# Kernel optimization log

Hardware: AMD Instinct MI355X
Metric: run time of the kernel (lower is better)

The kernel has to match this reference:

```python
import jax, jax.numpy as jnp
import numpy as np

D_MODEL = 192
D_STATE = 16
D_CONV = 3
EXPAND = 2
D_INNER = EXPAND * D_MODEL  # 384
DT_RANK = (D_MODEL + 15) // 16  # 12
K = 4  # scan directions
B, H, W = 2, 64, 64
EPS = 1e-5


def silu(x):
    return x * jax.nn.sigmoid(x)


def setup_inputs() -> dict:
    key = jax.random.key(0)
    ks = jax.random.split(key, 12)
    s = 0.02
    x = jax.random.normal(ks[0], (B, H, W, D_MODEL), dtype=jnp.float32)
    in_proj_w = jax.random.normal(ks[1], (2 * D_INNER, D_MODEL), dtype=jnp.float32) * s
    conv_w = jax.random.normal(ks[2], (D_INNER, 1, D_CONV, D_CONV), dtype=jnp.float32) * 0.1
    conv_b = jnp.zeros((D_INNER,), dtype=jnp.float32)
    x_proj_weight = jax.random.normal(ks[3], (K, DT_RANK + 2 * D_STATE, D_INNER), dtype=jnp.float32) * s
    dt_projs_weight = jax.random.normal(ks[4], (K, D_INNER, DT_RANK), dtype=jnp.float32) * (DT_RANK ** -0.5)
    dt_projs_bias = jax.random.uniform(ks[5], (K, D_INNER), dtype=jnp.float32, minval=-4.0, maxval=-2.0)
    # Mamba-style S4D-real init: A_n = n, stored as log
    A_logs = jnp.log(jnp.tile(jnp.arange(1, D_STATE + 1, dtype=jnp.float32), (K * D_INNER, 1)))
    Ds = jnp.ones((K * D_INNER,), dtype=jnp.float32)
    ln_gamma = jnp.ones((D_INNER,), dtype=jnp.float32)
    ln_beta = jnp.zeros((D_INNER,), dtype=jnp.float32)
    out_proj_w = jax.random.normal(ks[6], (D_MODEL, D_INNER), dtype=jnp.float32) * s
    return dict(x=x, in_proj_w=in_proj_w, conv_w=conv_w, conv_b=conv_b,
                x_proj_weight=x_proj_weight, dt_projs_weight=dt_projs_weight,
                dt_projs_bias=dt_projs_bias, A_logs=A_logs, Ds=Ds,
                ln_gamma=ln_gamma, ln_beta=ln_beta, out_proj_w=out_proj_w)


def _ss2d_forward(x, in_proj_w, conv_w, conv_b, x_proj_weight, dt_projs_weight,
                  dt_projs_bias, A_logs, Ds, ln_gamma, ln_beta, out_proj_w):
    b, h, w, _ = x.shape
    L = h * w
    # in_proj + gate split
    xz = jnp.einsum('bhwc,dc->bhwd', x, in_proj_w)  # (B,H,W,2*D_INNER)
    xc, z = jnp.split(xz, 2, axis=-1)
    # depthwise conv2d (NCHW) + SiLU
    xc = jnp.transpose(xc, (0, 3, 1, 2))  # (B,D_INNER,H,W)
    xc = jax.lax.conv_general_dilated(
        xc, conv_w, window_strides=(1, 1), padding=((1, 1), (1, 1)),
        feature_group_count=D_INNER, dimension_numbers=('NCHW', 'OIHW', 'NCHW'))
    xc = silu(xc + conv_b[None, :, None, None])
    # ---- cross-scan: 4 directions ----
    x_flat = xc.reshape(b, D_INNER, L)                                # HW order
    x_t = jnp.transpose(xc, (0, 1, 3, 2)).reshape(b, D_INNER, L)      # WH order
    xs = jnp.stack([x_flat, x_t], axis=1)                             # (B,2,D,L)
    xs = jnp.concatenate([xs, jnp.flip(xs, axis=-1)], axis=1)         # (B,4,D,L)
    # input-dependent projections
    x_dbl = jnp.einsum('bkdl,kcd->bkcl', xs, x_proj_weight)
    dts = x_dbl[:, :, :DT_RANK]
    Bmat = x_dbl[:, :, DT_RANK:DT_RANK + D_STATE]                     # (B,4,N,L)
    Cmat = x_dbl[:, :, DT_RANK + D_STATE:]                            # (B,4,N,L)
    dts = jnp.einsum('bkrl,kdr->bkdl', dts, dt_projs_weight)          # (B,4,D,L)
    delta = jax.nn.softplus(dts + dt_projs_bias[None, :, :, None])
    A = -jnp.exp(A_logs).reshape(K, D_INNER, D_STATE)                 # (4,D,N)
    # ---- selective scan over L (time-major) ----
    u_t = jnp.transpose(xs, (3, 0, 1, 2))        # (L,B,4,D)
    d_t = jnp.transpose(delta, (3, 0, 1, 2))     # (L,B,4,D)
    B_t = jnp.transpose(Bmat, (3, 0, 1, 2))      # (L,B,4,N)
    C_t = jnp.transpose(Cmat, (3, 0, 1, 2))      # (L,B,4,N)

    def step(hst, inp):
        d, bm, cm, uu = inp                       # (B,4,D) / (B,4,N)
        dA = jnp.exp(d[..., None] * A[None])      # (B,4,D,N)
        dBu = (d * uu)[..., None] * bm[:, :, None, :]
        hst = dA * hst + dBu
        y = jnp.einsum('bkdn,bkn->bkd', hst, cm)
        return hst, y

    h0 = jnp.zeros((b, K, D_INNER, D_STATE), dtype=x.dtype)
    _, ys = jax.lax.scan(step, h0, (d_t, B_t, C_t, u_t))              # (L,B,4,D)
    ys = jnp.transpose(ys, (1, 2, 3, 0))                              # (B,4,D,L)
    ys = ys + xs * Ds.reshape(K, D_INNER)[None, :, :, None]
    # ---- cross-merge ----
    y1 = ys[:, 0]
    inv2 = jnp.flip(ys[:, 2], axis=-1)
    wh = jnp.transpose(ys[:, 1].reshape(b, D_INNER, w, h), (0, 1, 3, 2)).reshape(b, D_INNER, L)
    invwh = jnp.transpose(jnp.flip(ys[:, 3], axis=-1).reshape(b, D_INNER, w, h), (0, 1, 3, 2)).reshape(b, D_INNER, L)
    y = y1 + inv2 + wh + invwh                                        # (B,D,L)
    y = jnp.transpose(y, (0, 2, 1)).reshape(b, h, w, D_INNER)
    # LayerNorm over channel
    mu = jnp.mean(y, axis=-1, keepdims=True)
    var = jnp.var(y, axis=-1, keepdims=True)
    y = (y - mu) * jax.lax.rsqrt(var + EPS) * ln_gamma + ln_beta
    # gate + out_proj
    y = y * silu(z)
    return jnp.einsum('bhwd,cd->bhwc', y, out_proj_w)


def reference(x, in_proj_w, conv_w, conv_b, x_proj_weight, dt_projs_weight,
              dt_projs_bias, A_logs, Ds, ln_gamma, ln_beta, out_proj_w):
    return _ss2d_forward(x, in_proj_w, conv_w, conv_b, x_proj_weight,
                         dt_projs_weight, dt_projs_bias, A_logs, Ds,
                         ln_gamma, ln_beta, out_proj_w)
```

## Files before the change

### kernel.cpp

```cpp
#include <hip/hip_runtime.h>
#include <cstddef>
#include <cstdint>

#define L 4096
#define DI 384
#define NDIR 4
#define NST 16
#define NCH 128
#define LCH 32
#define DTR 12

typedef __attribute__((ext_vector_type(8))) short bf16x8;
typedef __attribute__((ext_vector_type(4))) float f32x4;
typedef __attribute__((ext_vector_type(2))) float f32x2;

__device__ __forceinline__ unsigned short f2bf(float f) {
  unsigned u = __float_as_uint(f);
  u = u + 0x7fffu + ((u >> 16) & 1u);
  return (unsigned short)(u >> 16);
}
__device__ __forceinline__ float bf2f(unsigned short s) {
  return __uint_as_float(((unsigned)s) << 16);
}

__global__ __launch_bounds__(256) void cvt_all(
    const float* __restrict__ x, const float* __restrict__ ipw,
    const float* __restrict__ xpw, const float* __restrict__ opw,
    unsigned short* __restrict__ xb, unsigned short* __restrict__ ib,
    unsigned short* __restrict__ pb, unsigned short* __restrict__ ob) {
  int g = blockIdx.x * 256 + threadIdx.x;
  const float* src;
  unsigned short* dst;
  int idx;
  if (g < 393216) { src = x; dst = xb; idx = g; }
  else if (g < 430080) { src = ipw; dst = ib; idx = g - 393216; }
  else if (g < 446976) { src = xpw; dst = pb; idx = g - 430080; }
  else { src = opw; dst = ob; idx = g - 446976; }
  float4 v = *(const float4*)(src + (size_t)idx * 4);
  *(uint2*)(dst + (size_t)idx * 4) = make_uint2(
      (unsigned)f2bf(v.x) | ((unsigned)f2bf(v.y) << 16),
      (unsigned)f2bf(v.z) | ((unsigned)f2bf(v.w) << 16));
}

__global__ __launch_bounds__(256) void inproj_mfma(
    const unsigned short* __restrict__ A, const unsigned short* __restrict__ Bw,
    unsigned short* __restrict__ xc, unsigned short* __restrict__ z) {
  __shared__ unsigned short As[128 * 64];
  __shared__ unsigned short Bs[64 * 64];
  const int tid = threadIdx.x;
  const int m0 = blockIdx.x << 7;
  const int n0 = blockIdx.y << 6;
  const int lr = tid >> 4;
  const int lc = (tid & 15) << 2;
  const int wid = tid >> 6;
  const int lane = tid & 63;
  const int wr = wid >> 1, wc = wid & 1;
  const int Kdim = 192;
  f32x4 acc[4][2] = {};
  for (int k0 = 0; k0 < Kdim; k0 += 64) {
    if (k0) __syncthreads();
#pragma unroll
    for (int rr = 0; rr < 8; ++rr) {
      int r = lr + (rr << 4);
      uint2 v = *(const uint2*)(A + (size_t)(m0 + r) * Kdim + k0 + lc);
      unsigned off = ((unsigned)(r * 128 + lc * 2)) ^ ((r & 7) << 4);
      *(uint2*)((char*)As + off) = v;
    }
#pragma unroll
    for (int rr = 0; rr < 4; ++rr) {
      int r = lr + (rr << 4);
      uint2 v = *(const uint2*)(Bw + (size_t)(n0 + r) * Kdim + k0 + lc);
      unsigned off = ((unsigned)(r * 128 + lc * 2)) ^ ((r & 7) << 4);
      *(uint2*)((char*)Bs + off) = v;
    }
    __syncthreads();
#pragma unroll
    for (int kt = 0; kt < 2; ++kt) {
      const int kb = (kt << 6) + ((lane >> 4) << 4);
      bf16x8 af[4], bfr[2];
#pragma unroll
      for (int fr = 0; fr < 4; ++fr) {
        int row = (wr << 6) + (fr << 4) + (lane & 15);
        unsigned off = ((unsigned)(row * 128 + kb)) ^ ((row & 7) << 4);
        af[fr] = *(const bf16x8*)((const char*)As + off);
      }
#pragma unroll
      for (int fc = 0; fc < 2; ++fc) {
        int row = (wc << 5) + (fc << 4) + (lane & 15);
        unsigned off = ((unsigned)(row * 128 + kb)) ^ ((row & 7) << 4);
        bfr[fc] = *(const bf16x8*)((const char*)Bs + off);
      }
#pragma unroll
      for (int fr = 0; fr < 4; ++fr)
#pragma unroll
        for (int fc = 0; fc < 2; ++fc)
          acc[fr][fc] = __builtin_amdgcn_mfma_f32_16x16x32_bf16(af[fr], bfr[fc], acc[fr][fc], 0, 0, 0);
    }
  }
  const int rbase = (lane >> 4) << 2;
  const int cbase = lane & 15;
#pragma unroll
  for (int fr = 0; fr < 4; ++fr) {
#pragma unroll
    for (int fc = 0; fc < 2; ++fc) {
      int col = n0 + (wc << 5) + (fc << 4) + cbase;
      unsigned short* dst = xc;
      int cc = col;
      if (col >= 384) { dst = z; cc = col - 384; }
#pragma unroll
      for (int i = 0; i < 4; ++i) {
        int row = m0 + (wr << 6) + (fr << 4) + rbase + i;
        dst[(size_t)row * 384 + cc] = f2bf(acc[fr][fc][i]);
      }
    }
  }
}

__global__ __launch_bounds__(256) void gemm_nt_mfma_bfA(
    const unsigned short* __restrict__ A, const unsigned short* __restrict__ Bw,
    float* __restrict__ out0, int Kdim, int Ntot) {
  __shared__ unsigned short As[128 * 64];
  __shared__ unsigned short Bs[64 * 64];
  const int tid = threadIdx.x;
  const int m0 = blockIdx.x << 7;
  const int n0 = blockIdx.y << 6;
  const int lr = tid >> 4;
  const int lc = (tid & 15) << 2;
  const int wid = tid >> 6;
  const int lane = tid & 63;
  const int wr = wid >> 1, wc = wid & 1;
  f32x4 acc[4][2] = {};
  for (int k0 = 0; k0 < Kdim; k0 += 64) {
    if (k0) __syncthreads();
#pragma unroll
    for (int rr = 0; rr < 8; ++rr) {
      int r = lr + (rr << 4);
      uint2 v = *(const uint2*)(A + (size_t)(m0 + r) * Kdim + k0 + lc);
      unsigned off = ((unsigned)(r * 128 + lc * 2)) ^ ((r & 7) << 4);
      *(uint2*)((char*)As + off) = v;
    }
#pragma unroll
    for (int rr = 0; rr < 4; ++rr) {
      int r = lr + (rr << 4);
      uint2 v = *(const uint2*)(Bw + (size_t)(n0 + r) * Kdim + k0 + lc);
      unsigned off = ((unsigned)(r * 128 + lc * 2)) ^ ((r & 7) << 4);
      *(uint2*)((char*)Bs + off) = v;
    }
    __syncthreads();
#pragma unroll
    for (int kt = 0; kt < 2; ++kt) {
      const int kb = (kt << 6) + ((lane >> 4) << 4);
      bf16x8 af[4], bfr[2];
#pragma unroll
      for (int fr = 0; fr < 4; ++fr) {
        int row = (wr << 6) + (fr << 4) + (lane & 15);
        unsigned off = ((unsigned)(row * 128 + kb)) ^ ((row & 7) << 4);
        af[fr] = *(const bf16x8*)((const char*)As + off);
      }
#pragma unroll
      for (int fc = 0; fc < 2; ++fc) {
        int row = (wc << 5) + (fc << 4) + (lane & 15);
        unsigned off = ((unsigned)(row * 128 + kb)) ^ ((row & 7) << 4);
        bfr[fc] = *(const bf16x8*)((const char*)Bs + off);
      }
#pragma unroll
      for (int fr = 0; fr < 4; ++fr)
#pragma unroll
        for (int fc = 0; fc < 2; ++fc)
          acc[fr][fc] = __builtin_amdgcn_mfma_f32_16x16x32_bf16(af[fr], bfr[fc], acc[fr][fc], 0, 0, 0);
    }
  }
  const int rbase = (lane >> 4) << 2;
  const int cbase = lane & 15;
#pragma unroll
  for (int fr = 0; fr < 4; ++fr) {
#pragma unroll
    for (int fc = 0; fc < 2; ++fc) {
      int col = n0 + (wc << 5) + (fc << 4) + cbase;
#pragma unroll
      for (int i = 0; i < 4; ++i) {
        int row = m0 + (wr << 6) + (fr << 4) + rbase + i;
        out0[(size_t)row * Ntot + col] = acc[fr][fc][i];
      }
    }
  }
}

__global__ __launch_bounds__(384) void conv_silu(
    const unsigned short* __restrict__ xc_pre, const float* __restrict__ conv_w,
    const float* __restrict__ conv_b, unsigned short* __restrict__ xc_act,
    unsigned short* __restrict__ xc_act_t) {
  const int d = threadIdx.x;
  float w[9];
#pragma unroll
  for (int j = 0; j < 9; ++j) w[j] = conv_w[d * 9 + j];
  const float bias = conv_b[d];
  const int base = blockIdx.x << 2;
#pragma unroll
  for (int t = 0; t < 4; ++t) {
    int g = base + t;
    int b = g >> 12;
    int hw = g & 4095;
    int h = hw >> 6, ww = hw & 63;
    float s = bias;
#pragma unroll
    for (int ky = 0; ky < 3; ++ky) {
      int hh = h + ky - 1;
      if (hh < 0 || hh > 63) continue;
#pragma unroll
      for (int kx = 0; kx < 3; ++kx) {
        int wc = ww + kx - 1;
        if (wc < 0 || wc > 63) continue;
        s += w[ky * 3 + kx] * bf2f(xc_pre[((size_t)(b << 12) + (hh << 6) + wc) * DI + d]);
      }
    }
    float va = s / (1.f + __expf(-s));
    unsigned short vb = f2bf(va);
    xc_act[(size_t)g * DI + d] = vb;
    xc_act_t[((size_t)(b << 12) + (ww << 6) + h) * DI + d] = vb;
  }
}

__global__ __launch_bounds__(256) void xdbl_mfma(
    const unsigned short* __restrict__ xc_act, const unsigned short* __restrict__ xc_act_t,
    const unsigned short* __restrict__ xpw, float* __restrict__ xdbl) {
  __shared__ unsigned short As[128 * 64];
  __shared__ unsigned short Bs[48 * 64];
  const int tid = threadIdx.x;
  const int k = blockIdx.y, b = blockIdx.z;
  const int l0 = blockIdx.x << 7;
  const int bk = b * NDIR + k;
  const int lr = tid >> 4;
  const int lc = (tid & 15) << 2;
  const int wid = tid >> 6;
  const int lane = tid & 63;
  const unsigned short* usrc = (k & 1) ? xc_act_t : xc_act;
  const unsigned short* wbase = xpw + (size_t)k * 44 * DI;
  f32x4 acc[2][3] = {};
  for (int k0 = 0; k0 < DI; k0 += 64) {
    if (k0) __syncthreads();
#pragma unroll
    for (int rr = 0; rr < 8; ++rr) {
      int r = lr + (rr << 4);
      int l = l0 + r;
      int ll = (k & 2) ? (L - 1 - l) : l;
      uint2 v = *(const uint2*)(usrc + ((size_t)(b << 12) + ll) * DI + k0 + lc);
      unsigned off = ((unsigned)(r * 128 + lc * 2)) ^ ((r & 7) << 4);
      *(uint2*)((char*)As + off) = v;
    }
#pragma unroll
    for (int rr = 0; rr < 3; ++rr) {
      int r = lr + (rr << 4);
      uint2 v = make_uint2(0u, 0u);
      if (r < 44) v = *(const uint2*)(wbase + (size_t)r * DI + k0 + lc);
      unsigned off = ((unsigned)(r * 128 + lc * 2)) ^ ((r & 7) << 4);
      *(uint2*)((char*)Bs + off) = v;
    }
    __syncthreads();
#pragma unroll
    for (int kt = 0; kt < 2; ++kt) {
      const int kb = (kt << 6) + ((lane >> 4) << 4);
      bf16x8 af[2], bfr[3];
#pragma unroll
      for (int fr = 0; fr < 2; ++fr) {
        int row = (wid << 5) + (fr << 4) + (lane & 15);
        unsigned off = ((unsigned)(row * 128 + kb)) ^ ((row & 7) << 4);
        af[fr] = *(const bf16x8*)((const char*)As + off);
      }
#pragma unroll
      for (int nf = 0; nf < 3; ++nf) {
        int row = (nf << 4) + (lane & 15);
        unsigned off = ((unsigned)(row * 128 + kb)) ^ ((row & 7) << 4);
        bfr[nf] = *(const bf16x8*)((const char*)Bs + off);
      }
#pragma unroll
      for (int fr = 0; fr < 2; ++fr)
#pragma unroll
        for (int nf = 0; nf < 3; ++nf)
          acc[fr][nf] = __builtin_amdgcn_mfma_f32_16x16x32_bf16(af[fr], bfr[nf], acc[fr][nf], 0, 0, 0);
    }
  }
  const int rbase = (lane >> 4) << 2;
  const int cbase = lane & 15;
#pragma unroll
  for (int fr = 0; fr < 2; ++fr) {
#pragma unroll
    for (int nf = 0; nf < 3; ++nf) {
      int n = (nf << 4) + cbase;
#pragma unroll
      for (int i = 0; i < 4; ++i) {
        int row = l0 + (wid << 5) + (fr << 4) + rbase + i;
        xdbl[((size_t)bk * L + row) * 48 + n] = acc[fr][nf][i];
      }
    }
  }
}

__device__ __forceinline__ float delta_dot2(const float* __restrict__ Xrow,
                                            const f32x2* w2, float bias) {
  f32x2 acc = {bias, 0.f};
#pragma unroll
  for (int r = 0; r < 6; ++r) {
    f32x2 t = *(const f32x2*)(Xrow + 2 * r);
    acc = t * w2[r] + acc;
  }
  return acc.x + acc.y;
}

__device__ __forceinline__ void h_update4(f32x4* h4, const float* __restrict__ Brow,
                                          float p, float du) {
  float q2 = p * p, q4 = q2 * q2, q8 = q4 * q4;
  f32x4 e0;
  e0.x = p; e0.y = q2; e0.z = q2 * p; e0.w = q4;
  f32x4 e1 = e0 * q4, e2 = e0 * q8, e3 = e1 * q8;
  f32x4 B0 = *(const f32x4*)(Brow);
  f32x4 B1 = *(const f32x4*)(Brow + 4);
  f32x4 B2 = *(const f32x4*)(Brow + 8);
  f32x4 B3 = *(const f32x4*)(Brow + 12);
  h4[0] = e0 * h4[0] + du * B0;
  h4[1] = e1 * h4[1] + du * B1;
  h4[2] = e2 * h4[2] + du * B2;
  h4[3] = e3 * h4[3] + du * B3;
}

__global__ __launch_bounds__(192, 6) void scan_p1(
    const float* __restrict__ xdbl, const unsigned short* __restrict__ xc_act,
    const unsigned short* __restrict__ xc_act_t,
    const float* __restrict__ dtw, const float* __restrict__ dtb,
    unsigned short* __restrict__ ch_h, float* __restrict__ ch_sd,
    _Float16* __restrict__ cum, unsigned short* __restrict__ y_sc) {
  const int dh = blockIdx.z & 1;
  const int b = blockIdx.z >> 1;
  const int d = threadIdx.x + (dh ? 192 : 0);
  const int c = blockIdx.x, k = blockIdx.y;
  const int bk = b * NDIR + k;
  const float* xrow = xdbl + ((size_t)bk * L + c * LCH) * 48;
  f32x2 w2[6];
#pragma unroll
  for (int r = 0; r < 6; ++r) w2[r] = *(const f32x2*)(dtw + ((size_t)k * DI + d) * DTR + 2 * r);
  const float bias = dtb[k * DI + d];
  const unsigned short* usrc = (k & 1) ? xc_act_t : xc_act;
  const int ll0 = (k & 2) ? (L - 1 - c * LCH) : (c * LCH);
  const ptrdiff_t ustride = (k & 2) ? -(ptrdiff_t)DI : (ptrdiff_t)DI;
  const unsigned short* uptr = usrc + ((size_t)(b << 12) + ll0) * DI + d;
  _Float16* cbase = cum + ((size_t)bk * L + c * LCH) * DI + d;
  unsigned short* ybase = y_sc + ((size_t)bk * L + c * LCH) * DI + d;
  f32x4 h4[4] = {};
  float sd = 0.f;
  for (int g = 0; g < LCH; g += 4) {
    float du[4], p[4], dv4[4];
#pragma unroll
    for (int j = 0; j < 4; ++j) {
      int i = g + j;
      float a = delta_dot2(xrow + i * 48, w2, bias);
      float e = __expf(a);
      float dv = (a > 15.f) ? a : __logf(1.f + e);
      float u = bf2f(uptr[(ptrdiff_t)i * ustride]);
      dv4[j] = dv;
      p[j] = __builtin_amdgcn_rcpf(1.f + e);
      du[j] = dv * u;
    }
#pragma unroll
    for (int j = 0; j < 4; ++j) {
      int i = g + j;
      sd += dv4[j];
      cbase[(size_t)i * DI] = (_Float16)sd;
      h_update4(h4, xrow + i * 48 + DTR, p[j], du[j]);
      const float* Crow = xrow + i * 48 + DTR + NST;
      f32x4 y4 = h4[0] * (*(const f32x4*)(Crow));
      y4 = h4[1] * (*(const f32x4*)(Crow + 4)) + y4;
      y4 = h4[2] * (*(const f32x4*)(Crow + 8)) + y4;
      y4 = h4[3] * (*(const f32x4*)(Crow + 12)) + y4;
      ybase[(size_t)i * DI] = f2bf((y4.x + y4.y) + (y4.z + y4.w));
    }
  }
  size_t o = ((size_t)bk * NCH + c) * DI + d;
  ch_sd[o] = sd;
  const float* hf = (const float*)h4;
  unsigned wpk[8];
#pragma unroll
  for (int j = 0; j < 8; ++j)
    wpk[j] = (unsigned)f2bf(hf[2 * j]) | ((unsigned)f2bf(hf[2 * j + 1]) << 16);
  *(uint4*)(ch_h + o * 16) = make_uint4(wpk[0], wpk[1], wpk[2], wpk[3]);
  *(uint4*)(ch_h + o * 16 + 8) = make_uint4(wpk[4], wpk[5], wpk[6], wpk[7]);
}

__global__ __launch_bounds__(256) void scan_p2(
    const unsigned short* __restrict__ ch_h, const float* __restrict__ ch_sd,
    unsigned short* __restrict__ h0) {
  const int t = threadIdx.x;
  const int n = t & 15;
  const int dl = (t >> 4) & 3;
  const int seg = t >> 6;
  const int dg = blockIdx.x % 96;
  const int bk = blockIdx.x / 96;
  const int d = dg * 4 + dl;
  const float an = -(float)(n + 1);
  const int c0 = seg * 32;
  float carry = 0.f;
  float sdsum = 0.f;
  for (int i = 0; i < 32; ++i) {
    size_t o = ((size_t)bk * NCH + c0 + i) * DI + d;
    float sd = ch_sd[o];
    float hh = bf2f(ch_h[o * 16 + n]);
    carry = fmaf(__expf(an * sd), carry, hh);
    sdsum += sd;
  }
  __shared__ float sH[256], sS[256];
  sH[t] = carry;
  sS[t] = sdsum;
  __syncthreads();
  float E = 0.f;
  const int base = t & 63;
  for (int s = 0; s < seg; ++s) {
    float Rp = __expf(an * sS[base + 64 * s]);
    E = fmaf(Rp, E, sH[base + 64 * s]);
  }
  carry = E;
  for (int i = 0; i < 32; ++i) {
    size_t o = ((size_t)bk * NCH + c0 + i) * DI + d;
    float sd = ch_sd[o];
    float hh = bf2f(ch_h[o * 16 + n]);
    h0[o * 16 + n] = f2bf(carry);
    carry = fmaf(__expf(an * sd), carry, hh);
  }
}

__global__ __launch_bounds__(384) void merge_ln(
    const unsigned short* __restrict__ y_sc, const unsigned short* __restrict__ xc_act,
    const float* __restrict__ xdbl, const _Float16* __restrict__ cum,
    const unsigned short* __restrict__ h0,
    const float* __restrict__ Ds, const float* __restrict__ gamma,
    const float* __restrict__ beta, const unsigned short* __restrict__ z,
    unsigned short* __restrict__ y_gb) {
  const int d = threadIdx.x;
  const int g = blockIdx.x;
  const int b = g >> 12;
  const int hw = g & 4095;
  const int l1 = ((hw & 63) << 6) | (hw >> 6);
  const int ls[4] = {hw, l1, L - 1 - hw, L - 1 - l1};
  float v = 0.f;
#pragma unroll
  for (int k = 0; k < 4; ++k) {
    const int bk = b * NDIR + k;
    const int lk = ls[k];
    const size_t rowi = (size_t)bk * L + lk;
    float yl = bf2f(y_sc[rowi * DI + d]);
    float cs = (float)cum[rowi * DI + d];
    const float* Crow = xdbl + rowi * 48 + DTR + NST;
    const int c = lk >> 5;
    f32x4 hv[4];
    {
      const unsigned* hp = (const unsigned*)h0 + (((size_t)bk * NCH + c) * DI + d) * 8;
      float* hf = (float*)hv;
#pragma unroll
      for (int j = 0; j < 8; ++j) {
        unsigned u = hp[j];
        hf[2 * j] = bf2f((unsigned short)(u & 0xffffu));
        hf[2 * j + 1] = bf2f((unsigned short)(u >> 16));
      }
    }
    float q1 = __expf(-cs);
    float q2 = q1 * q1, q4 = q2 * q2, q8 = q4 * q4;
    f32x4 e0;
    e0.x = q1; e0.y = q2; e0.z = q2 * q1; e0.w = q4;
    f32x4 e1 = e0 * q4, e2 = e0 * q8, e3 = e1 * q8;
    f32x4 yv = (e0 * hv[0]) * (*(const f32x4*)(Crow));
    yv = (e1 * hv[1]) * (*(const f32x4*)(Crow + 4)) + yv;
    yv = (e2 * hv[2]) * (*(const f32x4*)(Crow + 8)) + yv;
    yv = (e3 * hv[3]) * (*(const f32x4*)(Crow + 12)) + yv;
    v += yl + ((yv.x + yv.y) + (yv.z + yv.w));
  }
  float u = bf2f(xc_act[(size_t)g * DI + d]);
  v += u * (Ds[d] + Ds[DI + d] + Ds[2 * DI + d] + Ds[3 * DI + d]);
  float s1 = v, s2 = v * v;
#pragma unroll
  for (int m = 1; m < 64; m <<= 1) {
    s1 += __shfl_xor(s1, m);
    s2 += __shfl_xor(s2, m);
  }
  __shared__ float r1[6], r2[6];
  const int lane = d & 63, wid = d >> 6;
  if (lane == 0) { r1[wid] = s1; r2[wid] = s2; }
  __syncthreads();
  float t1 = 0.f, t2 = 0.f;
#pragma unroll
  for (int wq = 0; wq < 6; ++wq) { t1 += r1[wq]; t2 += r2[wq]; }
  const float mu = t1 * (1.f / 384.f);
  const float var = t2 * (1.f / 384.f) - mu * mu;
  float yn = (v - mu) * rsqrtf(var + 1e-5f) * gamma[d] + beta[d];
  float zv = bf2f(z[(size_t)g * DI + d]);
  y_gb[(size_t)g * DI + d] = f2bf(yn * (zv / (1.f + __expf(-zv))));
}

extern "C" void kernel_launch(void* const* d_in, const int* in_sizes, int n_in,
                              void* d_out, int out_size, void* d_ws, size_t ws_size,
                              hipStream_t stream) {
  (void)in_sizes; (void)n_in; (void)out_size; (void)ws_size;
  const float* x      = (const float*)d_in[0];
  const float* ipw    = (const float*)d_in[1];
  const float* convw  = (const float*)d_in[2];
  const float* convb  = (const float*)d_in[3];
  const float* xpw    = (const float*)d_in[4];
  const float* dtw    = (const float*)d_in[5];
  const float* dtb    = (const float*)d_in[6];
  const float* Ds     = (const float*)d_in[8];
  const float* gamma  = (const float*)d_in[9];
  const float* beta   = (const float*)d_in[10];
  const float* opw    = (const float*)d_in[11];
  float* out = (float*)d_out;

  float* ws = (float*)d_ws;
  unsigned short* xc_pre   = (unsigned short*)ws;
  unsigned short* zbuf     = (unsigned short*)(ws + 1572864ull);
  unsigned short* xc_act   = (unsigned short*)(ws + 3145728ull);
  unsigned short* xc_act_t = (unsigned short*)(ws + 4718592ull);
  float* xdbl     = ws + 6291456ull;
  unsigned short* y_sc = (unsigned short*)(ws + 7864320ull);
  unsigned short* ch_h = (unsigned short*)(ws + 14155776ull);
  unsigned short* h0   = (unsigned short*)(ws + 17301504ull);
  float* ch_sd    = ws + 20447232ull;
  unsigned short* x_bf   = (unsigned short*)(ws + 20840448ull);
  unsigned short* ipw_bf = (unsigned short*)(ws + 21626880ull);
  unsigned short* xpw_bf = (unsigned short*)(ws + 21700608ull);
  unsigned short* opw_bf = (unsigned short*)(ws + 21734400ull);
  _Float16* cum   = (_Float16*)(ws + 21771264ull);
  unsigned short* y_gb = xc_pre;

  cvt_all<<<1818, 256, 0, stream>>>(x, ipw, xpw, opw, x_bf, ipw_bf, xpw_bf, opw_bf);
  inproj_mfma<<<dim3(64, 12), 256, 0, stream>>>(x_bf, ipw_bf, xc_pre, zbuf);
  conv_silu<<<2048, 384, 0, stream>>>(xc_pre, convw, convb, xc_act, xc_act_t);
  xdbl_mfma<<<dim3(32, 4, 2), 256, 0, stream>>>(xc_act, xc_act_t, xpw_bf, xdbl);
  scan_p1<<<dim3(NCH, 4, 4), 192, 0, stream>>>(xdbl, xc_act, xc_act_t, dtw, dtb, ch_h, ch_sd, cum, y_sc);
  scan_p2<<<768, 256, 0, stream>>>(ch_h, ch_sd, h0);
  merge_ln<<<8192, 384, 0, stream>>>(y_sc, xc_act, xdbl, cum, h0, Ds, gamma, beta, zbuf, y_gb);
  gemm_nt_mfma_bfA<<<dim3(64, 3), 256, 0, stream>>>(y_gb, opw_bf, out, 384, 192);
}
```

Before: 137.9 us.

## Fuse merge/LayerNorm/gate with out_proj GEMM and drop transposed activation copy

Merges the four-direction merge, LayerNorm and SiLU gate with the output projection in one kernel. Each block handles 32 rows held in shared memory and applies MFMA against the out_proj weights. It also removes the transposed activation buffer and reads the original layout with transposed indexing in xdbl and the scan. This cuts a kernel launch and the y_gb and xc_act_t round trips through memory. In exchange the grid is much smaller, with large LDS use and serial per-row work inside each block, and the scan reads become strided.

```diff
diff --git a/kernel.cpp b/kernel.cpp
--- a/kernel.cpp
+++ b/kernel.cpp
@@ -116,80 +116,9 @@
   }
 }
 
-__global__ __launch_bounds__(256) void gemm_nt_mfma_bfA(
-    const unsigned short* __restrict__ A, const unsigned short* __restrict__ Bw,
-    float* __restrict__ out0, int Kdim, int Ntot) {
-  __shared__ unsigned short As[128 * 64];
-  __shared__ unsigned short Bs[64 * 64];
-  const int tid = threadIdx.x;
-  const int m0 = blockIdx.x << 7;
-  const int n0 = blockIdx.y << 6;
-  const int lr = tid >> 4;
-  const int lc = (tid & 15) << 2;
-  const int wid = tid >> 6;
-  const int lane = tid & 63;
-  const int wr = wid >> 1, wc = wid & 1;
-  f32x4 acc[4][2] = {};
-  for (int k0 = 0; k0 < Kdim; k0 += 64) {
-    if (k0) __syncthreads();
-#pragma unroll
-    for (int rr = 0; rr < 8; ++rr) {
-      int r = lr + (rr << 4);
-      uint2 v = *(const uint2*)(A + (size_t)(m0 + r) * Kdim + k0 + lc);
-      unsigned off = ((unsigned)(r * 128 + lc * 2)) ^ ((r & 7) << 4);
-      *(uint2*)((char*)As + off) = v;
-    }
-#pragma unroll
-    for (int rr = 0; rr < 4; ++rr) {
-      int r = lr + (rr << 4);
-      uint2 v = *(const uint2*)(Bw + (size_t)(n0 + r) * Kdim + k0 + lc);
-      unsigned off = ((unsigned)(r * 128 + lc * 2)) ^ ((r & 7) << 4);
-      *(uint2*)((char*)Bs + off) = v;
-    }
-    __syncthreads();
-#pragma unroll
-    for (int kt = 0; kt < 2; ++kt) {
-      const int kb = (kt << 6) + ((lane >> 4) << 4);
-      bf16x8 af[4], bfr[2];
-#pragma unroll
-      for (int fr = 0; fr < 4; ++fr) {
-        int row = (wr << 6) + (fr << 4) + (lane & 15);
-        unsigned off = ((unsigned)(row * 128 + kb)) ^ ((row & 7) << 4);
-        af[fr] = *(const bf16x8*)((const char*)As + off);
-      }
-#pragma unroll
-      for (int fc = 0; fc < 2; ++fc) {
-        int row = (wc << 5) + (fc << 4) + (lane & 15);
-        unsigned off = ((unsigned)(row * 128 + kb)) ^ ((row & 7) << 4);
-        bfr[fc] = *(const bf16x8*)((const char*)Bs + off);
-      }
-#pragma unroll
-      for (int fr = 0; fr < 4; ++fr)
-#pragma unroll
-        for (int fc = 0; fc < 2; ++fc)
-          acc[fr][fc] = __builtin_amdgcn_mfma_f32_16x16x32_bf16(af[fr], bfr[fc], acc[fr][fc], 0, 0, 0);
-    }
-  }
-  const int rbase = (lane >> 4) << 2;
-  const int cbase = lane & 15;
-#pragma unroll
-  for (int fr = 0; fr < 4; ++fr) {
-#pragma unroll
-    for (int fc = 0; fc < 2; ++fc) {
-      int col = n0 + (wc << 5) + (fc << 4) + cbase;
-#pragma unroll
-      for (int i = 0; i < 4; ++i) {
-        int row = m0 + (wr << 6) + (fr << 4) + rbase + i;
-        out0[(size_t)row * Ntot + col] = acc[fr][fc][i];
-      }
-    }
-  }
-}
-
 __global__ __launch_bounds__(384) void conv_silu(
     const unsigned short* __restrict__ xc_pre, const float* __restrict__ conv_w,
-    const float* __restrict__ conv_b, unsigned short* __restrict__ xc_act,
-    unsigned short* __restrict__ xc_act_t) {
+    const float* __restrict__ conv_b, unsigned short* __restrict__ xc_act) {
   const int d = threadIdx.x;
   float w[9];
 #pragma unroll
@@ -215,14 +144,12 @@
       }
     }
     float va = s / (1.f + __expf(-s));
-    unsigned short vb = f2bf(va);
-    xc_act[(size_t)g * DI + d] = vb;
-    xc_act_t[((size_t)(b << 12) + (ww << 6) + h) * DI + d] = vb;
+    xc_act[(size_t)g * DI + d] = f2bf(va);
   }
 }
 
 __global__ __launch_bounds__(256) void xdbl_mfma(
-    const unsigned short* __restrict__ xc_act, const unsigned short* __restrict__ xc_act_t,
+    const unsigned short* __restrict__ xc_act,
     const unsigned short* __restrict__ xpw, float* __restrict__ xdbl) {
   __shared__ unsigned short As[128 * 64];
   __shared__ unsigned short Bs[48 * 64];
@@ -234,7 +161,6 @@
   const int lc = (tid & 15) << 2;
   const int wid = tid >> 6;
   const int lane = tid & 63;
-  const unsigned short* usrc = (k & 1) ? xc_act_t : xc_act;
   const unsigned short* wbase = xpw + (size_t)k * 44 * DI;
   f32x4 acc[2][3] = {};
   for (int k0 = 0; k0 < DI; k0 += 64) {
@@ -244,7 +170,8 @@
       int r = lr + (rr << 4);
       int l = l0 + r;
       int ll = (k & 2) ? (L - 1 - l) : l;
-      uint2 v = *(const uint2*)(usrc + ((size_t)(b << 12) + ll) * DI + k0 + lc);
+      if (k & 1) ll = ((ll & 63) << 6) | (ll >> 6);
+      uint2 v = *(const uint2*)(xc_act + ((size_t)(b << 12) + ll) * DI + k0 + lc);
       unsigned off = ((unsigned)(r * 128 + lc * 2)) ^ ((r & 7) << 4);
       *(uint2*)((char*)As + off) = v;
     }
@@ -325,7 +252,6 @@
 
 __global__ __launch_bounds__(192, 6) void scan_p1(
     const float* __restrict__ xdbl, const unsigned short* __restrict__ xc_act,
-    const unsigned short* __restrict__ xc_act_t,
     const float* __restrict__ dtw, const float* __restrict__ dtb,
     unsigned short* __restrict__ ch_h, float* __restrict__ ch_sd,
     _Float16* __restrict__ cum, unsigned short* __restrict__ y_sc) {
@@ -339,10 +265,11 @@
 #pragma unroll
   for (int r = 0; r < 6; ++r) w2[r] = *(const f32x2*)(dtw + ((size_t)k * DI + d) * DTR + 2 * r);
   const float bias = dtb[k * DI + d];
-  const unsigned short* usrc = (k & 1) ? xc_act_t : xc_act;
   const int ll0 = (k & 2) ? (L - 1 - c * LCH) : (c * LCH);
-  const ptrdiff_t ustride = (k & 2) ? -(ptrdiff_t)DI : (ptrdiff_t)DI;
-  const unsigned short* uptr = usrc + ((size_t)(b << 12) + ll0) * DI + d;
+  const int hw0 = (k & 1) ? (((ll0 & 63) << 6) | (ll0 >> 6)) : ll0;
+  ptrdiff_t ust = (k & 1) ? (ptrdiff_t)(64 * DI) : (ptrdiff_t)DI;
+  if (k & 2) ust = -ust;
+  const unsigned short* uptr = xc_act + ((size_t)(b << 12) + hw0) * DI + d;
   _Float16* cbase = cum + ((size_t)bk * L + c * LCH) * DI + d;
   unsigned short* ybase = y_sc + ((size_t)bk * L + c * LCH) * DI + d;
   f32x4 h4[4] = {};
@@ -355,7 +282,7 @@
       float a = delta_dot2(xrow + i * 48, w2, bias);
       float e = __expf(a);
       float dv = (a > 15.f) ? a : __logf(1.f + e);
-      float u = bf2f(uptr[(ptrdiff_t)i * ustride]);
+      float u = bf2f(uptr[(ptrdiff_t)i * ust]);
       dv4[j] = dv;
       p[j] = __builtin_amdgcn_rcpf(1.f + e);
       du[j] = dv * u;
@@ -426,71 +353,154 @@
   }
 }
 
-__global__ __launch_bounds__(384) void merge_ln(
+__global__ __launch_bounds__(384) void merge_out(
     const unsigned short* __restrict__ y_sc, const unsigned short* __restrict__ xc_act,
     const float* __restrict__ xdbl, const _Float16* __restrict__ cum,
     const unsigned short* __restrict__ h0,
     const float* __restrict__ Ds, const float* __restrict__ gamma,
     const float* __restrict__ beta, const unsigned short* __restrict__ z,
-    unsigned short* __restrict__ y_gb) {
+    const unsigned short* __restrict__ opw, float* __restrict__ out0) {
+  __shared__ unsigned short As6[6 * 32 * 64];
+  __shared__ unsigned short Bs[192 * 64];
+  __shared__ float vs[32 * DI];
+  __shared__ float r1s[32][6], r2s[32][6];
+  __shared__ float mus[32], rss[32];
   const int d = threadIdx.x;
-  const int g = blockIdx.x;
-  const int b = g >> 12;
-  const int hw = g & 4095;
-  const int l1 = ((hw & 63) << 6) | (hw >> 6);
-  const int ls[4] = {hw, l1, L - 1 - hw, L - 1 - l1};
-  float v = 0.f;
-#pragma unroll
-  for (int k = 0; k < 4; ++k) {
-    const int bk = b * NDIR + k;
-    const int lk = ls[k];
-    const size_t rowi = (size_t)bk * L + lk;
-    float yl = bf2f(y_sc[rowi * DI + d]);
-    float cs = (float)cum[rowi * DI + d];
-    const float* Crow = xdbl + rowi * 48 + DTR + NST;
-    const int c = lk >> 5;
-    f32x4 hv[4];
-    {
-      const unsigned* hp = (const unsigned*)h0 + (((size_t)bk * NCH + c) * DI + d) * 8;
-      float* hf = (float*)hv;
-#pragma unroll
-      for (int j = 0; j < 8; ++j) {
-        unsigned u = hp[j];
-        hf[2 * j] = bf2f((unsigned short)(u & 0xffffu));
-        hf[2 * j + 1] = bf2f((unsigned short)(u >> 16));
-      }
-    }
-    float q1 = __expf(-cs);
-    float q2 = q1 * q1, q4 = q2 * q2, q8 = q4 * q4;
-    f32x4 e0;
-    e0.x = q1; e0.y = q2; e0.z = q2 * q1; e0.w = q4;
-    f32x4 e1 = e0 * q4, e2 = e0 * q8, e3 = e1 * q8;
-    f32x4 yv = (e0 * hv[0]) * (*(const f32x4*)(Crow));
-    yv = (e1 * hv[1]) * (*(const f32x4*)(Crow + 4)) + yv;
-    yv = (e2 * hv[2]) * (*(const f32x4*)(Crow + 8)) + yv;
-    yv = (e3 * hv[3]) * (*(const f32x4*)(Crow + 12)) + yv;
-    v += yl + ((yv.x + yv.y) + (yv.z + yv.w));
-  }
-  float u = bf2f(xc_act[(size_t)g * DI + d]);
-  v += u * (Ds[d] + Ds[DI + d] + Ds[2 * DI + d] + Ds[3 * DI + d]);
-  float s1 = v, s2 = v * v;
-#pragma unroll
-  for (int m = 1; m < 64; m <<= 1) {
-    s1 += __shfl_xor(s1, m);
-    s2 += __shfl_xor(s2, m);
-  }
-  __shared__ float r1[6], r2[6];
+  const int b = blockIdx.x >> 7;
+  const int hw0 = (blockIdx.x & 127) << 5;
+  const int g0 = (b << 12) + hw0;
+  const float gam = gamma[d], bet = beta[d];
+  const float dsum = Ds[d] + Ds[DI + d] + Ds[2 * DI + d] + Ds[3 * DI + d];
+  f32x4 hv0[4], hv2[4];
+  {
+    const unsigned* hp = (const unsigned*)h0 +
+        (((size_t)((b << 2) + 0) * NCH + (hw0 >> 5)) * DI + d) * 8;
+    const unsigned* hp2 = (const unsigned*)h0 +
+        (((size_t)((b << 2) + 2) * NCH + (127 - (hw0 >> 5))) * DI + d) * 8;
+    float* hf = (float*)hv0;
+    float* hf2 = (float*)hv2;
+#pragma unroll
+    for (int j = 0; j < 8; ++j) {
+      unsigned u = hp[j], u2 = hp2[j];
+      hf[2 * j] = bf2f((unsigned short)(u & 0xffffu));
+      hf[2 * j + 1] = bf2f((unsigned short)(u >> 16));
+      hf2[2 * j] = bf2f((unsigned short)(u2 & 0xffffu));
+      hf2[2 * j + 1] = bf2f((unsigned short)(u2 >> 16));
+    }
+  }
   const int lane = d & 63, wid = d >> 6;
-  if (lane == 0) { r1[wid] = s1; r2[wid] = s2; }
+  for (int r = 0; r < 32; ++r) {
+    const int hw = hw0 + r;
+    const int l1 = ((hw & 63) << 6) | (hw >> 6);
+    const int ls[4] = {hw, l1, L - 1 - hw, L - 1 - l1};
+    float v = 0.f;
+#pragma unroll
+    for (int k = 0; k < 4; ++k) {
+      const int bk = (b << 2) + k;
+      const int lk = ls[k];
+      const size_t rowi = (size_t)bk * L + lk;
+      float yl = bf2f(y_sc[rowi * DI + d]);
+      float cs = (float)cum[rowi * DI + d];
+      const float* Crow = xdbl + rowi * 48 + DTR + NST;
+      f32x4 hv[4];
+      if (k & 1) {
+        const int c = lk >> 5;
+        const unsigned* hp = (const unsigned*)h0 + (((size_t)bk * NCH + c) * DI + d) * 8;
+        float* hf = (float*)hv;
+#pragma unroll
+        for (int j = 0; j < 8; ++j) {
+          unsigned u = hp[j];
+          hf[2 * j] = bf2f((unsigned short)(u & 0xffffu));
+          hf[2 * j + 1] = bf2f((unsigned short)(u >> 16));
+        }
+      } else {
+        const f32x4* src = (k == 0) ? hv0 : hv2;
+        hv[0] = src[0]; hv[1] = src[1]; hv[2] = src[2]; hv[3] = src[3];
+      }
+      float q1 = __expf(-cs);
+      float q2 = q1 * q1, q4 = q2 * q2, q8 = q4 * q4;
+      f32x4 e0;
+      e0.x = q1; e0.y = q2; e0.z = q2 * q1; e0.w = q4;
+      f32x4 e1 = e0 * q4, e2 = e0 * q8, e3 = e1 * q8;
+      f32x4 yv = (e0 * hv[0]) * (*(const f32x4*)(Crow));
+      yv = (e1 * hv[1]) * (*(const f32x4*)(Crow + 4)) + yv;
+      yv = (e2 * hv[2]) * (*(const f32x4*)(Crow + 8)) + yv;
+      yv = (e3 * hv[3]) * (*(const f32x4*)(Crow + 12)) + yv;
+      v += yl + ((yv.x + yv.y) + (yv.z + yv.w));
+    }
+    float u = bf2f(xc_act[(size_t)(g0 + r) * DI + d]);
+    v += u * dsum;
+    vs[r * DI + d] = v;
+    float s1 = v, s2 = v * v;
+#pragma unroll
+    for (int m = 1; m < 64; m <<= 1) {
+      s1 += __shfl_xor(s1, m);
+      s2 += __shfl_xor(s2, m);
+    }
+    if (lane == 0) { r1s[r][wid] = s1; r2s[r][wid] = s2; }
+  }
   __syncthreads();
-  float t1 = 0.f, t2 = 0.f;
-#pragma unroll
-  for (int wq = 0; wq < 6; ++wq) { t1 += r1[wq]; t2 += r2[wq]; }
-  const float mu = t1 * (1.f / 384.f);
-  const float var = t2 * (1.f / 384.f) - mu * mu;
-  float yn = (v - mu) * rsqrtf(var + 1e-5f) * gamma[d] + beta[d];
-  float zv = bf2f(z[(size_t)g * DI + d]);
-  y_gb[(size_t)g * DI + d] = f2bf(yn * (zv / (1.f + __expf(-zv))));
+  if (d < 32) {
+    float t1 = 0.f, t2 = 0.f;
+#pragma unroll
+    for (int wq = 0; wq < 6; ++wq) { t1 += r1s[d][wq]; t2 += r2s[d][wq]; }
+    const float mu = t1 * (1.f / 384.f);
+    const float var = t2 * (1.f / 384.f) - mu * mu;
+    mus[d] = mu;
+    rss[d] = rsqrtf(var + 1e-5f);
+  }
+  __syncthreads();
+  for (int r = 0; r < 32; ++r) {
+    float yn = (vs[r * DI + d] - mus[r]) * rss[r] * gam + bet;
+    float zv = bf2f(z[(size_t)(g0 + r) * DI + d]);
+    unsigned short yb = f2bf(yn * (zv / (1.f + __expf(-zv))));
+    unsigned off = ((unsigned)(r * 128 + (d & 63) * 2)) ^ ((r & 7) << 4);
+    *(unsigned short*)((char*)As6 + (d >> 6) * 4096 + off) = yb;
+  }
+  __syncthreads();
+  const int mh = wid & 1, nb = wid >> 1;
+  const int lr = d >> 4;
+  const int lc = (d & 15) << 2;
+  f32x4 acc[4] = {};
+  for (int k0 = 0; k0 < 6; ++k0) {
+    if (k0) __syncthreads();
+#pragma unroll
+    for (int rr = 0; rr < 8; ++rr) {
+      int r = lr + rr * 24;
+      uint2 v = *(const uint2*)(opw + (size_t)r * DI + k0 * 64 + lc);
+      unsigned off = ((unsigned)(r * 128 + lc * 2)) ^ ((r & 7) << 4);
+      *(uint2*)((char*)Bs + off) = v;
+    }
+    __syncthreads();
+#pragma unroll
+    for (int kt = 0; kt < 2; ++kt) {
+      const int kb = (kt << 6) + ((lane >> 4) << 4);
+      bf16x8 af;
+      {
+        int row = (mh << 4) + (lane & 15);
+        unsigned off = ((unsigned)(row * 128 + kb)) ^ ((row & 7) << 4);
+        af = *(const bf16x8*)((const char*)As6 + k0 * 4096 + off);
+      }
+#pragma unroll
+      for (int fc = 0; fc < 4; ++fc) {
+        int rowb = (nb << 6) + (fc << 4) + (lane & 15);
+        unsigned offb = ((unsigned)(rowb * 128 + kb)) ^ ((rowb & 7) << 4);
+        bf16x8 bf8 = *(const bf16x8*)((const char*)Bs + offb);
+        acc[fc] = __builtin_amdgcn_mfma_f32_16x16x32_bf16(af, bf8, acc[fc], 0, 0, 0);
+      }
+    }
+  }
+  const int rbase = (lane >> 4) << 2;
+  const int cbase = lane & 15;
+#pragma unroll
+  for (int fc = 0; fc < 4; ++fc) {
+    int col = (nb << 6) + (fc << 4) + cbase;
+#pragma unroll
+    for (int i = 0; i < 4; ++i) {
+      int row = g0 + (mh << 4) + rbase + i;
+      out0[(size_t)row * 192 + col] = acc[fc][i];
+    }
+  }
 }
 
 extern "C" void kernel_launch(void* const* d_in, const int* in_sizes, int n_in,
@@ -514,7 +524,6 @@
   unsigned short* xc_pre   = (unsigned short*)ws;
   unsigned short* zbuf     = (unsigned short*)(ws + 1572864ull);
   unsigned short* xc_act   = (unsigned short*)(ws + 3145728ull);
-  unsigned short* xc_act_t = (unsigned short*)(ws + 4718592ull);
   float* xdbl     = ws + 6291456ull;
   unsigned short* y_sc = (unsigned short*)(ws + 7864320ull);
   unsigned short* ch_h = (unsigned short*)(ws + 14155776ull);
@@ -525,14 +534,12 @@
   unsigned short* xpw_bf = (unsigned short*)(ws + 21700608ull);
   unsigned short* opw_bf = (unsigned short*)(ws + 21734400ull);
   _Float16* cum   = (_Float16*)(ws + 21771264ull);
-  unsigned short* y_gb = xc_pre;
 
   cvt_all<<<1818, 256, 0, stream>>>(x, ipw, xpw, opw, x_bf, ipw_bf, xpw_bf, opw_bf);
   inproj_mfma<<<dim3(64, 12), 256, 0, stream>>>(x_bf, ipw_bf, xc_pre, zbuf);
-  conv_silu<<<2048, 384, 0, stream>>>(xc_pre, convw, convb, xc_act, xc_act_t);
-  xdbl_mfma<<<dim3(32, 4, 2), 256, 0, stream>>>(xc_act, xc_act_t, xpw_bf, xdbl);
-  scan_p1<<<dim3(NCH, 4, 4), 192, 0, stream>>>(xdbl, xc_act, xc_act_t, dtw, dtb, ch_h, ch_sd, cum, y_sc);
+  conv_silu<<<2048, 384, 0, stream>>>(xc_pre, convw, convb, xc_act);
+  xdbl_mfma<<<dim3(32, 4, 2), 256, 0, stream>>>(xc_act, xpw_bf, xdbl);
+  scan_p1<<<dim3(NCH, 4, 4), 192, 0, stream>>>(xdbl, xc_act, dtw, dtb, ch_h, ch_sd, cum, y_sc);
   scan_p2<<<768, 256, 0, stream>>>(ch_h, ch_sd, h0);
-  merge_ln<<<8192, 384, 0, stream>>>(y_sc, xc_act, xdbl, cum, h0, Ds, gamma, beta, zbuf, y_gb);
-  gemm_nt_mfma_bfA<<<dim3(64, 3), 256, 0, stream>>>(y_gb, opw_bf, out, 384, 192);
-}
+  merge_out<<<256, 384, 0, stream>>>(y_sc, xc_act, xdbl, cum, h0, Ds, gamma, beta, zbuf, opw_bf, out);
+}
```

After: 158.9 us. 15.2% more time.
